# Kernel tuning notes

Measured on AMD Instinct MI355X. Metric: run time of the kernel, lower is better.

Reference implementation:

```python
import jax, jax.numpy as jnp
import numpy as np


def cayley_batch(data):
    # data: (b, r, r). Q = (I + skew) @ (I - skew)^{-1}  (torch solve with left=False)
    b, rr, _ = data.shape
    skew = 0.5 * (data - data.transpose(0, 2, 1))
    I = jnp.eye(rr, dtype=data.dtype)
    A = I - skew  # always invertible (skew-symmetric)
    B = I + skew
    # Solve X @ A = B  ->  A^T X^T = B^T
    Q = jnp.linalg.solve(A.transpose(0, 2, 1), B.transpose(0, 2, 1)).transpose(0, 2, 1)
    return Q


def blockdiag_butterfly_multiply(x, w1, w2):
    # x: (batch, n); w1: (k, q, p) with k*p == n; w2: (l, s, r) with l*r == k*q
    batch = x.shape[0]
    k, q, p = w1.shape
    l, s, r = w2.shape
    out1 = jnp.einsum('bkp,kqp->bkq', x.reshape(batch, k, p), w1)  # (batch, k, q)
    # flat (k*q) viewed as (r, l), then transposed -> (batch, l, r)
    out1 = out1.reshape(batch, r, l).transpose(0, 2, 1)
    out2 = jnp.einsum('blr,lsr->bls', out1, w2)  # (batch, l, s)
    # permute to (batch, s, l) and flatten -> (batch, s*l)
    return out2.transpose(0, 2, 1).reshape(batch, s * l)


def setup_inputs() -> dict:
    key = jax.random.key(0)
    k1, k2, k3 = jax.random.split(key, 3)
    n, nblocks = 4096, 64
    bs = n // nblocks  # 64
    x = jax.random.normal(k1, (16384, n), dtype=jnp.float32)
    L = jax.random.normal(k2, (nblocks, bs, bs), dtype=jnp.float32)
    R = jax.random.normal(k3, (nblocks, bs, bs), dtype=jnp.float32)
    return {"x": x, "L": L, "R": R}


def reference(x, L, R):
    # GSOrthogonal.forward with orthogonal=True, method='cayley':
    # orthogonalize L and R, then butterfly multiply with (x, R_orth, L_orth)
    Lq = cayley_batch(L)
    Rq = cayley_batch(R)
    return blockdiag_butterfly_multiply(x, Rq, Lq)
```

## Files before the change

### kernel.cpp

```cpp
#include <hip/hip_runtime.h>
#include <hip/hip_bf16.h>

typedef __bf16 bf16x4 __attribute__((ext_vector_type(4)));
typedef __bf16 bf16x8 __attribute__((ext_vector_type(8)));
typedef float  floatx4 __attribute__((ext_vector_type(4)));

__global__ __launch_bounds__(256) void cayley_pack_kernel(
    const float* __restrict__ L, const float* __restrict__ R,
    __bf16* __restrict__ ws) {
  __shared__ float Ms[64][65];
  __shared__ float Pa[2][64];
  __shared__ float Pi[2][64];
  __shared__ float fcol[2][64];

  const int blk = blockIdx.x;
  const int t = threadIdx.x;
  const float* M = (blk < 64) ? (R + (size_t)blk * 4096)
                              : (L + (size_t)(blk - 64) * 4096);
  __bf16* dst = ws + (size_t)blk * 4096;

  for (int u = 0; u < 16; ++u) {
    int idx = u * 256 + t;
    Ms[idx >> 6][idx & 63] = M[idx];
  }
  __syncthreads();

  const int i = t >> 2;
  const int g = t & 3;
  const int jb = g * 16;
  float a[16], v[16];
#pragma unroll
  for (int jj = 0; jj < 16; ++jj) {
    int j = jb + jj;
    float s = 0.5f * (Ms[i][j] - Ms[j][i]);
    a[jj] = (i == j ? 1.0f : 0.0f) - s;
    v[jj] = (i == j ? 1.0f : 0.0f);
  }
  __syncthreads();

#pragma unroll 4
  for (int k = 0; k < 64; ++k) {
    const int kb = k & 1;
    if (g == (k >> 4)) fcol[kb][i] = a[k & 15];
    if (i == k) {
#pragma unroll
      for (int jj = 0; jj < 16; ++jj) { Pa[kb][jb + jj] = a[jj]; Pi[kb][jb + jj] = v[jj]; }
    }
    __syncthreads();
    const float ip = 1.0f / Pa[kb][k];
    if (i == k) {
#pragma unroll
      for (int jj = 0; jj < 16; ++jj) { a[jj] *= ip; v[jj] *= ip; }
    } else {
      const float f = fcol[kb][i] * ip;
#pragma unroll
      for (int jj = 0; jj < 16; ++jj) {
        a[jj] -= f * Pa[kb][jb + jj];
        v[jj] -= f * Pi[kb][jb + jj];
      }
    }
  }

#pragma unroll
  for (int jj = 0; jj < 16; ++jj) {
    int j = jb + jj;
    Ms[i][j] = 2.0f * v[jj] - (i == j ? 1.0f : 0.0f);
  }
  __syncthreads();

  const int lane = t & 63;
  const int grp = t >> 6;
  const int colq = lane & 15;
  const int quad = lane >> 4;
#pragma unroll
  for (int kh = 0; kh < 2; ++kh) {
    bf16x8 pk;
#pragma unroll
    for (int j8 = 0; j8 < 8; ++j8)
      pk[j8] = (__bf16)Ms[16 * grp + colq][32 * kh + 8 * quad + j8];
    *(bf16x8*)(dst + (kh * 4 + grp) * 512 + lane * 8) = pk;
  }
}

__global__ __launch_bounds__(512, 2) void butterfly_kernel(
    const float* __restrict__ x, const __bf16* __restrict__ ws,
    float* __restrict__ out) {
  extern __shared__ short interS[];
  __bf16* inter = (__bf16*)interS;

  const int t = threadIdx.x;
  const int wv = t >> 6;
  const int lane = t & 63;
  const int col = lane & 15;
  const int quad = lane >> 4;
  const size_t b0 = (size_t)blockIdx.x * 16;

  const __bf16* w1 = ws;
  const __bf16* w2 = ws + 64 * 4096;

  const float* xrow = x + (b0 + (size_t)col) * 4096;
#pragma unroll
  for (int rg = 0; rg < 2; ++rg) {
    const int r0 = wv * 8 + rg * 4;
    bf16x8 afrag[4][2];
#pragma unroll
    for (int ir = 0; ir < 4; ++ir) {
      const float* src = xrow + (r0 + ir) * 64 + quad * 8;
#pragma unroll
      for (int kh = 0; kh < 2; ++kh) {
        floatx4 u = *(const floatx4*)(src + kh * 32);
        floatx4 w = *(const floatx4*)(src + kh * 32 + 4);
        bf16x8 f;
        f[0] = (__bf16)u[0]; f[1] = (__bf16)u[1];
        f[2] = (__bf16)u[2]; f[3] = (__bf16)u[3];
        f[4] = (__bf16)w[0]; f[5] = (__bf16)w[1];
        f[6] = (__bf16)w[2]; f[7] = (__bf16)w[3];
        afrag[ir][kh] = f;
      }
    }
#pragma unroll
    for (int qc = 0; qc < 4; ++qc) {
      floatx4 vals[4];
#pragma unroll
      for (int ir = 0; ir < 4; ++ir) {
        const int r = r0 + ir;
        bf16x8 bf0 = *(const bf16x8*)(w1 + (size_t)r * 4096 + (0 * 4 + qc) * 512 + lane * 8);
        bf16x8 bf1 = *(const bf16x8*)(w1 + (size_t)r * 4096 + (1 * 4 + qc) * 512 + lane * 8);
        floatx4 acc = {0.f, 0.f, 0.f, 0.f};
        acc = __builtin_amdgcn_mfma_f32_16x16x32_bf16(afrag[ir][0], bf0, acc, 0, 0, 0);
        acc = __builtin_amdgcn_mfma_f32_16x16x32_bf16(afrag[ir][1], bf1, acc, 0, 0, 0);
        vals[ir] = acc;
      }
      const int l = qc * 16 + col;
#pragma unroll
      for (int reg = 0; reg < 4; ++reg) {
        const int b = quad * 4 + reg;
        bf16x4 pk;
        pk[0] = (__bf16)vals[0][reg];
        pk[1] = (__bf16)vals[1][reg];
        pk[2] = (__bf16)vals[2][reg];
        pk[3] = (__bf16)vals[3][reg];
        const int cs = wv ^ (b & 7) ^ (l & 7);
        *(bf16x4*)(inter + l * 1024 + b * 64 + cs * 8 + rg * 4) = pk;
      }
    }
  }
  __syncthreads();

  const int wl = wv & 3;
  const int b = col;
  float* outb = out + b0 * 4096;
#pragma unroll
  for (int sci = 0; sci < 2; ++sci) {
    const int sc = (wv >> 2) * 2 + sci;
    floatx4 vals[16];
#pragma unroll
    for (int l16 = 0; l16 < 16; ++l16) {
      const int l = wl * 16 + l16;
      const int swz = (b & 7) ^ (l & 7);
      bf16x8 a0 = *(const bf16x8*)(inter + l * 1024 + b * 64 + (quad ^ swz) * 8);
      bf16x8 a1 = *(const bf16x8*)(inter + l * 1024 + b * 64 + ((4 + quad) ^ swz) * 8);
      bf16x8 bf0 = *(const bf16x8*)(w2 + (size_t)l * 4096 + (0 * 4 + sc) * 512 + lane * 8);
      bf16x8 bf1 = *(const bf16x8*)(w2 + (size_t)l * 4096 + (1 * 4 + sc) * 512 + lane * 8);
      floatx4 acc = {0.f, 0.f, 0.f, 0.f};
      acc = __builtin_amdgcn_mfma_f32_16x16x32_bf16(a0, bf0, acc, 0, 0, 0);
      acc = __builtin_amdgcn_mfma_f32_16x16x32_bf16(a1, bf1, acc, 0, 0, 0);
      vals[l16] = acc;
    }
    const int s = sc * 16 + col;
#pragma unroll
    for (int reg = 0; reg < 4; ++reg) {
      const int bb = quad * 4 + reg;
      float* dstp = outb + (size_t)bb * 4096 + s * 64 + wl * 16;
#pragma unroll
      for (int q4 = 0; q4 < 4; ++q4) {
        floatx4 vv;
        vv[0] = vals[q4 * 4 + 0][reg];
        vv[1] = vals[q4 * 4 + 1][reg];
        vv[2] = vals[q4 * 4 + 2][reg];
        vv[3] = vals[q4 * 4 + 3][reg];
        *(floatx4*)(dstp + q4 * 4) = vv;
      }
    }
  }
}

extern "C" void kernel_launch(void* const* d_in, const int* in_sizes, int n_in,
                              void* d_out, int out_size, void* d_ws, size_t ws_size,
                              hipStream_t stream) {
  const float* x = (const float*)d_in[0];
  const float* L = (const float*)d_in[1];
  const float* R = (const float*)d_in[2];
  float* out = (float*)d_out;
  __bf16* ws = (__bf16*)d_ws;

  const int nrows = in_sizes[0] / 4096;

  cayley_pack_kernel<<<128, 256, 0, stream>>>(L, R, ws);
  butterfly_kernel<<<nrows / 16, 512, 131072, stream>>>(x, ws, out);
}
```

Baseline: 605.5 us.

## Stage butterfly output through LDS for coalesced stores and double-buffer weight loads

The second stage is reorganised so each wave owns 8 l-blocks. Its A fragments are loaded into registers once, and the results are written into a swizzled LDS bounce buffer. From there each wave writes full contiguous output rows with coalesced 16-byte stores, where before each lane wrote scattered 64-byte pieces. Weight fragment loads in both stages are double-buffered in registers to overlap global loads with MFMA, and the unroll pragma on the Cayley elimination loop is removed. The cost is higher register pressure and extra barriers and LDS traffic per block.

```diff
diff --git a/kernel.cpp b/kernel.cpp
--- a/kernel.cpp
+++ b/kernel.cpp
@@ -38,7 +38,6 @@
   }
   __syncthreads();
 
-#pragma unroll 4
   for (int k = 0; k < 64; ++k) {
     const int kb = k & 1;
     if (g == (k >> 4)) fcol[kb][i] = a[k & 15];
@@ -87,6 +86,7 @@
     float* __restrict__ out) {
   extern __shared__ short interS[];
   __bf16* inter = (__bf16*)interS;
+  float* bounce = (float*)interS;
 
   const int t = threadIdx.x;
   const int wv = t >> 6;
@@ -102,33 +102,51 @@
 #pragma unroll
   for (int rg = 0; rg < 2; ++rg) {
     const int r0 = wv * 8 + rg * 4;
-    bf16x8 afrag[4][2];
+    floatx4 xu[4][2], xw[4][2];
 #pragma unroll
     for (int ir = 0; ir < 4; ++ir) {
       const float* src = xrow + (r0 + ir) * 64 + quad * 8;
 #pragma unroll
       for (int kh = 0; kh < 2; ++kh) {
-        floatx4 u = *(const floatx4*)(src + kh * 32);
-        floatx4 w = *(const floatx4*)(src + kh * 32 + 4);
+        xu[ir][kh] = *(const floatx4*)(src + kh * 32);
+        xw[ir][kh] = *(const floatx4*)(src + kh * 32 + 4);
+      }
+    }
+    bf16x8 wfr[2][4][2];
+#pragma unroll
+    for (int ir = 0; ir < 4; ++ir)
+#pragma unroll
+      for (int kh = 0; kh < 2; ++kh)
+        wfr[0][ir][kh] = *(const bf16x8*)(
+            w1 + (size_t)(r0 + ir) * 4096 + (kh * 4 + 0) * 512 + lane * 8);
+    bf16x8 af[4][2];
+#pragma unroll
+    for (int ir = 0; ir < 4; ++ir)
+#pragma unroll
+      for (int kh = 0; kh < 2; ++kh) {
         bf16x8 f;
-        f[0] = (__bf16)u[0]; f[1] = (__bf16)u[1];
-        f[2] = (__bf16)u[2]; f[3] = (__bf16)u[3];
-        f[4] = (__bf16)w[0]; f[5] = (__bf16)w[1];
-        f[6] = (__bf16)w[2]; f[7] = (__bf16)w[3];
-        afrag[ir][kh] = f;
-      }
-    }
+        f[0] = (__bf16)xu[ir][kh][0]; f[1] = (__bf16)xu[ir][kh][1];
+        f[2] = (__bf16)xu[ir][kh][2]; f[3] = (__bf16)xu[ir][kh][3];
+        f[4] = (__bf16)xw[ir][kh][0]; f[5] = (__bf16)xw[ir][kh][1];
+        f[6] = (__bf16)xw[ir][kh][2]; f[7] = (__bf16)xw[ir][kh][3];
+        af[ir][kh] = f;
+      }
 #pragma unroll
     for (int qc = 0; qc < 4; ++qc) {
+      if (qc < 3) {
+#pragma unroll
+        for (int ir = 0; ir < 4; ++ir)
+#pragma unroll
+          for (int kh = 0; kh < 2; ++kh)
+            wfr[(qc + 1) & 1][ir][kh] = *(const bf16x8*)(
+                w1 + (size_t)(r0 + ir) * 4096 + (kh * 4 + qc + 1) * 512 + lane * 8);
+      }
       floatx4 vals[4];
 #pragma unroll
       for (int ir = 0; ir < 4; ++ir) {
-        const int r = r0 + ir;
-        bf16x8 bf0 = *(const bf16x8*)(w1 + (size_t)r * 4096 + (0 * 4 + qc) * 512 + lane * 8);
-        bf16x8 bf1 = *(const bf16x8*)(w1 + (size_t)r * 4096 + (1 * 4 + qc) * 512 + lane * 8);
         floatx4 acc = {0.f, 0.f, 0.f, 0.f};
-        acc = __builtin_amdgcn_mfma_f32_16x16x32_bf16(afrag[ir][0], bf0, acc, 0, 0, 0);
-        acc = __builtin_amdgcn_mfma_f32_16x16x32_bf16(afrag[ir][1], bf1, acc, 0, 0, 0);
+        acc = __builtin_amdgcn_mfma_f32_16x16x32_bf16(af[ir][0], wfr[qc & 1][ir][0], acc, 0, 0, 0);
+        acc = __builtin_amdgcn_mfma_f32_16x16x32_bf16(af[ir][1], wfr[qc & 1][ir][1], acc, 0, 0, 0);
         vals[ir] = acc;
       }
       const int l = qc * 16 + col;
@@ -147,41 +165,75 @@
   }
   __syncthreads();
 
-  const int wl = wv & 3;
-  const int b = col;
+  bf16x8 A0[8], A1[8];
+#pragma unroll
+  for (int l16 = 0; l16 < 8; ++l16) {
+    const int l = wv * 8 + l16;
+    const int swz = (col & 7) ^ (l & 7);
+    A0[l16] = *(const bf16x8*)(inter + l * 1024 + col * 64 + (quad ^ swz) * 8);
+    A1[l16] = *(const bf16x8*)(inter + l * 1024 + col * 64 + ((4 + quad) ^ swz) * 8);
+  }
+  __syncthreads();
+
   float* outb = out + b0 * 4096;
 #pragma unroll
-  for (int sci = 0; sci < 2; ++sci) {
-    const int sc = (wv >> 2) * 2 + sci;
-    floatx4 vals[16];
-#pragma unroll
-    for (int l16 = 0; l16 < 16; ++l16) {
-      const int l = wl * 16 + l16;
-      const int swz = (b & 7) ^ (l & 7);
-      bf16x8 a0 = *(const bf16x8*)(inter + l * 1024 + b * 64 + (quad ^ swz) * 8);
-      bf16x8 a1 = *(const bf16x8*)(inter + l * 1024 + b * 64 + ((4 + quad) ^ swz) * 8);
-      bf16x8 bf0 = *(const bf16x8*)(w2 + (size_t)l * 4096 + (0 * 4 + sc) * 512 + lane * 8);
-      bf16x8 bf1 = *(const bf16x8*)(w2 + (size_t)l * 4096 + (1 * 4 + sc) * 512 + lane * 8);
-      floatx4 acc = {0.f, 0.f, 0.f, 0.f};
-      acc = __builtin_amdgcn_mfma_f32_16x16x32_bf16(a0, bf0, acc, 0, 0, 0);
-      acc = __builtin_amdgcn_mfma_f32_16x16x32_bf16(a1, bf1, acc, 0, 0, 0);
-      vals[l16] = acc;
-    }
-    const int s = sc * 16 + col;
-#pragma unroll
-    for (int reg = 0; reg < 4; ++reg) {
-      const int bb = quad * 4 + reg;
-      float* dstp = outb + (size_t)bb * 4096 + s * 64 + wl * 16;
-#pragma unroll
-      for (int q4 = 0; q4 < 4; ++q4) {
-        floatx4 vv;
-        vv[0] = vals[q4 * 4 + 0][reg];
-        vv[1] = vals[q4 * 4 + 1][reg];
-        vv[2] = vals[q4 * 4 + 2][reg];
-        vv[3] = vals[q4 * 4 + 3][reg];
-        *(floatx4*)(dstp + q4 * 4) = vv;
-      }
-    }
+  for (int p = 0; p < 2; ++p) {
+    bf16x8 wf2[2][2][2];
+#pragma unroll
+    for (int scloc = 0; scloc < 2; ++scloc)
+#pragma unroll
+      for (int kh = 0; kh < 2; ++kh)
+        wf2[0][scloc][kh] = *(const bf16x8*)(
+            w2 + (size_t)(wv * 8) * 4096 + (kh * 4 + p * 2 + scloc) * 512 + lane * 8);
+    floatx4 acc[8][2];
+#pragma unroll
+    for (int l16 = 0; l16 < 8; ++l16) {
+      if (l16 < 7) {
+        const int ln = wv * 8 + l16 + 1;
+#pragma unroll
+        for (int scloc = 0; scloc < 2; ++scloc)
+#pragma unroll
+          for (int kh = 0; kh < 2; ++kh)
+            wf2[(l16 + 1) & 1][scloc][kh] = *(const bf16x8*)(
+                w2 + (size_t)ln * 4096 + (kh * 4 + p * 2 + scloc) * 512 + lane * 8);
+      }
+#pragma unroll
+      for (int scloc = 0; scloc < 2; ++scloc) {
+        floatx4 a = {0.f, 0.f, 0.f, 0.f};
+        a = __builtin_amdgcn_mfma_f32_16x16x32_bf16(A0[l16], wf2[l16 & 1][scloc][0], a, 0, 0, 0);
+        a = __builtin_amdgcn_mfma_f32_16x16x32_bf16(A1[l16], wf2[l16 & 1][scloc][1], a, 0, 0, 0);
+        acc[l16][scloc] = a;
+      }
+    }
+#pragma unroll
+    for (int scloc = 0; scloc < 2; ++scloc)
+#pragma unroll
+      for (int reg = 0; reg < 4; ++reg)
+#pragma unroll
+        for (int h = 0; h < 2; ++h) {
+          const int b = quad * 4 + reg;
+          const int g = b * 512 + scloc * 256 + col * 16 + wv * 2 + h;
+          const int gp = g ^ ((g >> 4) & 7);
+          floatx4 pk;
+          pk[0] = acc[h * 4 + 0][scloc][reg];
+          pk[1] = acc[h * 4 + 1][scloc][reg];
+          pk[2] = acc[h * 4 + 2][scloc][reg];
+          pk[3] = acc[h * 4 + 3][scloc][reg];
+          *(floatx4*)(bounce + gp * 4) = pk;
+        }
+    __syncthreads();
+#pragma unroll
+    for (int rr = 0; rr < 2; ++rr) {
+      const int b = wv * 2 + rr;
+#pragma unroll
+      for (int i = 0; i < 8; ++i) {
+        const int g = b * 512 + i * 64 + lane;
+        const int gp = g ^ ((g >> 4) & 7);
+        floatx4 v = *(const floatx4*)(bounce + gp * 4);
+        *(floatx4*)(outb + (size_t)b * 4096 + p * 2048 + i * 256 + lane * 4) = v;
+      }
+    }
+    __syncthreads();
   }
 }
 
```

Result: faster. 522.2 us (-13.8%).
